# Performance work log

Measured on AMD Instinct MI355X. Metric: run time of the kernel, lower is better.

## Reference

```python
import jax, jax.numpy as jnp
import numpy as np

NUM_GRAPHS = 256


def _mean_aggregate(h, src, dst, num_nodes):
    # DGL copy_src + mean reduce: dst node gets mean of src-node features over in-edges.
    summed = jax.ops.segment_sum(h[src], dst, num_segments=num_nodes)  # [N, F]
    deg = jax.ops.segment_sum(jnp.ones((src.shape[0],), h.dtype), dst, num_segments=num_nodes)
    return summed / jnp.maximum(deg, 1.0)[:, None]


def setup_inputs() -> dict:
    key = jax.random.key(0)
    ks = jax.random.split(key, 10)
    N, E, D_IN, H1, H2, OUT = 50000, 800000, 128, 256, 128, 1
    s = lambda fan: 1.0 / np.sqrt(fan)
    return {
        "h": jax.random.normal(ks[0], (N, D_IN), jnp.float32),
        "src": jax.random.randint(ks[1], (E,), 0, N),
        "dst": jax.random.randint(ks[2], (E,), 0, N),
        "graph_ids": jnp.sort(jax.random.randint(ks[3], (N,), 0, NUM_GRAPHS)),
        "W1": jax.random.normal(ks[4], (D_IN, H1), jnp.float32) * s(D_IN),
        "b1": jnp.zeros((H1,), jnp.float32),
        "W2": jax.random.normal(ks[5], (H1, H1), jnp.float32) * s(H1),
        "b2": jnp.zeros((H1,), jnp.float32),
        "Wr1": jax.random.normal(ks[6], (H1, H2), jnp.float32) * s(H1),
        "br1": jnp.zeros((H2,), jnp.float32),
        "Wr2": jax.random.normal(ks[7], (H2, OUT), jnp.float32) * s(H2),
        "br2": jnp.zeros((OUT,), jnp.float32),
    }


def reference(h, src, dst, graph_ids, W1, b1, W2, b2, Wr1, br1, Wr2, br2):
    N = h.shape[0]
    # GCN layer 1: mean-aggregate then linear+ReLU
    h = _mean_aggregate(h, src, dst, N)
    h = jax.nn.relu(h @ W1 + b1)
    # GCN layer 2
    h = _mean_aggregate(h, src, dst, N)
    h = jax.nn.relu(h @ W2 + b2)
    # dgl.mean_nodes readout: per-graph mean of node features
    gsum = jax.ops.segment_sum(h, graph_ids, num_segments=NUM_GRAPHS)  # [G, H1]
    gcnt = jax.ops.segment_sum(jnp.ones((N,), h.dtype), graph_ids, num_segments=NUM_GRAPHS)
    hg = gsum / jnp.maximum(gcnt, 1.0)[:, None]
    hidden = hg @ Wr1 + br1
    return hidden @ Wr2 + br2  # [G, 1]
```

## Files before the change

kernel.cpp:

```cpp
#include <hip/hip_runtime.h>


#define NUM_GRAPHS 256
#define MAXDEG 64
#define GSHIFT 8
#define GCAP 4864
#define CHUNK_MAX 3200

#define PART_B0 0
#define PART_NB 256
#define CST_B0 (PART_B0 + PART_NB)
#define CST_NB 512
#define GST_B0 (CST_B0 + CST_NB)
#define GST_NB 64
#define WT1_B0 (GST_B0 + GST_NB)
#define WT1_NB 16
#define WT2_B0 (WT1_B0 + WT1_NB)
#define WT2_NB 32
#define MISC_NB (WT2_B0 + WT2_NB)

typedef __attribute__((ext_vector_type(8))) short bf16x8;
typedef __attribute__((ext_vector_type(4))) float f32x4;
typedef __attribute__((ext_vector_type(4))) unsigned int u32x4;

__device__ inline unsigned short f2bf(float f) {
    unsigned u = __float_as_uint(f);
    return (unsigned short)((u + 0x7fff + ((u >> 16) & 1)) >> 16);
}
__device__ inline float bflo(unsigned u) { return __uint_as_float(u << 16); }
__device__ inline float bfhi(unsigned u) { return __uint_as_float(u & 0xffff0000u); }


__launch_bounds__(256)
__global__ void misc_kernel(const int* __restrict__ dst, const int* __restrict__ src,
                            const int* __restrict__ gids,
                            const float* __restrict__ h,
                            const float* __restrict__ W1, const float* __restrict__ W2,
                            int* __restrict__ cursor, unsigned* __restrict__ partE,
                            int* __restrict__ gstart,
                            unsigned short* __restrict__ hb,
                            unsigned short* __restrict__ Wt1, unsigned short* __restrict__ Wt2,
                            int N, int E) {
    int b = blockIdx.x, tid = threadIdx.x;
    if (b < CST_B0) {
        __shared__ unsigned lcnt[256];
        __shared__ unsigned sbuf[256];
        __shared__ unsigned lbase[257];
        __shared__ unsigned gb[256];
        __shared__ unsigned comp[CHUNK_MAX];
        int b0 = b - PART_B0;
        int chunk = (E + PART_NB - 1) / PART_NB;
        int ebeg = b0 * chunk;
        int eend = ebeg + chunk; if (eend > E) eend = E;
        int ecount = eend - ebeg; if (ecount < 0) ecount = 0;

        lcnt[tid] = 0;
        __syncthreads();
        for (int e = ebeg + tid; e < eend; e += 256) {
            int d = __builtin_nontemporal_load(&dst[e]);
            atomicAdd(&lcnt[d >> GSHIFT], 1u);
        }
        __syncthreads();
        unsigned v = lcnt[tid];
        sbuf[tid] = v;
        __syncthreads();
        #pragma unroll
        for (int dd = 1; dd < 256; dd <<= 1) {
            unsigned t = (tid >= dd) ? sbuf[tid - dd] : 0u;
            __syncthreads();
            sbuf[tid] += t;
            __syncthreads();
        }
        lbase[tid] = sbuf[tid] - v;
        if (tid == 255) lbase[256] = sbuf[255];
        gb[tid] = v ? (unsigned)atomicAdd(&cursor[tid], (int)v) : 0u;
        lcnt[tid] = 0;
        __syncthreads();
        for (int e = ebeg + tid; e < eend; e += 256) {
            int d = __builtin_nontemporal_load(&dst[e]);
            int s = __builtin_nontemporal_load(&src[e]);
            int g = d >> GSHIFT;
            unsigned r = atomicAdd(&lcnt[g], 1u) + lbase[g];
            if (r < (unsigned)CHUNK_MAX)
                comp[r] = ((unsigned)s << GSHIFT) | (unsigned)(d & 255);
        }
        __syncthreads();
        for (int i = tid; i < ecount; i += 256) {
            int lo = 0, hi = 256;
            while (hi - lo > 1) {
                int mid = (lo + hi) >> 1;
                if (lbase[mid] <= (unsigned)i) lo = mid; else hi = mid;
            }
            unsigned dest = (unsigned)lo * GCAP + gb[lo] + ((unsigned)i - lbase[lo]);
            if (dest < (unsigned)(256 * GCAP))
                __builtin_nontemporal_store(comp[i], &partE[dest]);
        }
    } else if (b < GST_B0) {
        int lid = (b - CST_B0) * 256 + tid;
        int total4 = N * 32;
        for (int i = lid; i < total4; i += CST_NB * 256) {
            float4 v = *(const float4*)(h + (size_t)i * 4);
            ushort4 o;
            o.x = f2bf(v.x); o.y = f2bf(v.y); o.z = f2bf(v.z); o.w = f2bf(v.w);
            *(ushort4*)(hb + (size_t)i * 4) = o;
        }
    } else if (b < WT1_B0) {
        int lid = (b - GST_B0) * 256 + tid;
        for (int n = lid; n < N; n += GST_NB * 256) {
            int g = gids[n];
            int gp = (n == 0) ? -1 : gids[n - 1];
            for (int x = gp + 1; x <= g; ++x) gstart[x] = n;
            if (n == N - 1)
                for (int x = g + 1; x <= NUM_GRAPHS; ++x) gstart[x] = N;
        }
    } else if (b < WT2_B0) {
        int lid = (b - WT1_B0) * 256 + tid;
        for (int i = lid; i < 256 * 128; i += WT1_NB * 256)
            Wt1[i] = f2bf(W1[(size_t)(i & 127) * 256 + (i >> 7)]);
    } else {
        int lid = (b - WT2_B0) * 256 + tid;
        for (int i = lid; i < 256 * 256; i += WT2_NB * 256)
            Wt2[i] = f2bf(W2[(size_t)(i & 255) * 256 + (i >> 8)]);
    }
}


__launch_bounds__(256)
__global__ void build_kernel(const unsigned* __restrict__ partE,
                             const int* __restrict__ cursor,
                             int* __restrict__ cnt, unsigned short* __restrict__ eidx,
                             int N) {
    __shared__ unsigned short es[256 * MAXDEG];
    __shared__ unsigned hist[256];
    int g = blockIdx.x, tid = threadIdx.x;
    hist[tid] = 0;
    __syncthreads();
    int ec = cursor[g]; if (ec > GCAP) ec = GCAP;
    const unsigned* pe = partE + (size_t)g * GCAP;
    for (int i = tid; i < ec; i += 256) {
        unsigned p = pe[i];
        int dl = (int)(p & 255);
        int s = (int)(p >> GSHIFT);
        unsigned r = atomicAdd(&hist[dl], 1u);
        if (r < MAXDEG)
            es[dl * MAXDEG + r] = (unsigned short)s;
    }
    __syncthreads();
    const u32x4* s4 = (const u32x4*)es;
    u32x4* d4 = (u32x4*)(eidx + ((size_t)g << GSHIFT) * MAXDEG);
    for (int i = tid; i < 2048; i += 256)
        __builtin_nontemporal_store(s4[i], &d4[i]);
    int node = (g << GSHIFT) + tid;
    if (node < N) cnt[node] = (int)hist[tid];
}


template <int D>
__global__ void agg_mean_bf16_kernel(const unsigned short* __restrict__ feat,
                                     const int* __restrict__ cnt,
                                     const unsigned short* __restrict__ eidx,
                                     unsigned short* __restrict__ out, int N) {
    constexpr int VPL = D / 64;
    int wave = blockIdx.x * (blockDim.x >> 6) + (threadIdx.x >> 6);
    int lane = threadIdx.x & 63;
    if (wave >= N) return;
    int deg = cnt[wave];
    int stored = deg > MAXDEG ? MAXDEG : deg;
    const unsigned short* row = eidx + (size_t)wave * MAXDEG;
    int myIdx = (lane < stored) ? (int)row[lane] : 0;

    float acc[VPL];
    #pragma unroll
    for (int i = 0; i < VPL; ++i) acc[i] = 0.0f;

    int j = 0;
    for (; j + 8 <= stored; j += 8) {
        if constexpr (VPL == 2) {
            unsigned v[8];
            #pragma unroll
            for (int u = 0; u < 8; ++u) {
                int s = __shfl(myIdx, j + u, 64);
                v[u] = *(const unsigned*)(feat + (size_t)s * D + lane * 2);
            }
            #pragma unroll
            for (int u = 0; u < 8; ++u) { acc[0] += bflo(v[u]); acc[1] += bfhi(v[u]); }
        } else {
            uint2 v[8];
            #pragma unroll
            for (int u = 0; u < 8; ++u) {
                int s = __shfl(myIdx, j + u, 64);
                v[u] = *(const uint2*)(feat + (size_t)s * D + lane * 4);
            }
            #pragma unroll
            for (int u = 0; u < 8; ++u) {
                acc[0] += bflo(v[u].x); acc[1] += bfhi(v[u].x);
                acc[2] += bflo(v[u].y); acc[3] += bfhi(v[u].y);
            }
        }
    }
    for (; j < stored; ++j) {
        int s = __shfl(myIdx, j, 64);
        if constexpr (VPL == 2) {
            unsigned v = *(const unsigned*)(feat + (size_t)s * D + lane * 2);
            acc[0] += bflo(v); acc[1] += bfhi(v);
        } else {
            uint2 v = *(const uint2*)(feat + (size_t)s * D + lane * 4);
            acc[0] += bflo(v.x); acc[1] += bfhi(v.x);
            acc[2] += bflo(v.y); acc[3] += bfhi(v.y);
        }
    }

    float invd = 1.0f / (float)(deg > 0 ? deg : 1);
    if constexpr (VPL == 2) {
        unsigned o = (unsigned)f2bf(acc[0] * invd) | ((unsigned)f2bf(acc[1] * invd) << 16);
        __builtin_nontemporal_store(o, (unsigned*)(out + (size_t)wave * D + lane * 2));
    } else {
        unsigned lo = (unsigned)f2bf(acc[0] * invd) | ((unsigned)f2bf(acc[1] * invd) << 16);
        unsigned hi = (unsigned)f2bf(acc[2] * invd) | ((unsigned)f2bf(acc[3] * invd) << 16);
        unsigned long long o = (unsigned long long)lo | ((unsigned long long)hi << 32);
        __builtin_nontemporal_store(o, (unsigned long long*)(out + (size_t)wave * D + lane * 4));
    }
}


template <int K, int MODE>
__launch_bounds__(256)
__global__ void gemm_mfma_kernel(const unsigned short* __restrict__ A,
                                 const unsigned short* __restrict__ Wt,
                                 const float* __restrict__ bias,
                                 unsigned short* __restrict__ Cb,
                                 const int* __restrict__ gids,
                                 float* __restrict__ gsum,
                                 int N) {
    constexpr int LDS = 40;
    __shared__ unsigned short As[64 * LDS];
    __shared__ unsigned short Bs[256 * LDS];

    int tid = threadIdx.x;
    int wave = tid >> 6;
    int lane = tid & 63;
    int m = lane & 15;
    int q = lane >> 4;
    int rowBase = blockIdx.x * 64;

    f32x4 acc[4][4] = {};

    for (int kc = 0; kc < K; kc += 32) {
        {
            int r = tid >> 2;
            int seg = tid & 3;
            int gr = rowBase + r;
            uint4 v = make_uint4(0, 0, 0, 0);
            if (gr < N) v = *(const uint4*)(A + (size_t)gr * K + kc + seg * 8);
            *(uint4*)&As[r * LDS + seg * 8] = v;
        }
        #pragma unroll
        for (int it = 0; it < 4; ++it) {
            int n = (tid >> 2) + it * 64;
            int seg = tid & 3;
            uint4 v = *(const uint4*)(Wt + (size_t)n * K + kc + seg * 8);
            *(uint4*)&Bs[n * LDS + seg * 8] = v;
        }
        __syncthreads();

        bf16x8 af[4], bfr[4];
        #pragma unroll
        for (int r = 0; r < 4; ++r)
            af[r] = *(const bf16x8*)&As[(r * 16 + m) * LDS + q * 8];
        #pragma unroll
        for (int c = 0; c < 4; ++c)
            bfr[c] = *(const bf16x8*)&Bs[(wave * 64 + c * 16 + m) * LDS + q * 8];
        #pragma unroll
        for (int r = 0; r < 4; ++r)
            #pragma unroll
            for (int c = 0; c < 4; ++c)
                acc[r][c] = __builtin_amdgcn_mfma_f32_16x16x32_bf16(af[r], bfr[c], acc[r][c], 0, 0, 0);
        __syncthreads();
    }

    if constexpr (MODE == 0) {
        #pragma unroll
        for (int c = 0; c < 4; ++c) {
            int col = wave * 64 + c * 16 + m;
            float bv = bias[col];
            #pragma unroll
            for (int r = 0; r < 4; ++r) {
                #pragma unroll
                for (int reg = 0; reg < 4; ++reg) {
                    int grow = rowBase + r * 16 + q * 4 + reg;
                    if (grow < N)
                        Cb[(size_t)grow * 256 + col] = f2bf(fmaxf(acc[r][c][reg] + bv, 0.0f));
                }
            }
        }
    } else {
        int* sgid = (int*)As;
        if (tid < 64) {
            int gr = rowBase + tid;
            sgid[tid] = (gr < N) ? gids[gr] : 0x7fffffff;
        }
        __syncthreads();
        int lastValid = N - 1 - rowBase;
        if (lastValid > 63) lastValid = 63;
        int gmin = sgid[0];
        int gmax = sgid[lastValid];
        #pragma unroll
        for (int c = 0; c < 4; ++c) {
            int col = wave * 64 + c * 16 + m;
            float bv = bias[col];
            for (int g = gmin; g <= gmax; ++g) {
                float p = 0.0f;
                #pragma unroll
                for (int r = 0; r < 4; ++r) {
                    #pragma unroll
                    for (int reg = 0; reg < 4; ++reg) {
                        int lr = r * 16 + q * 4 + reg;
                        if (sgid[lr] == g)
                            p += fmaxf(acc[r][c][reg] + bv, 0.0f);
                    }
                }
                p += __shfl_xor(p, 16, 64);
                p += __shfl_xor(p, 32, 64);
                if (q == 0 && p != 0.0f)
                    atomicAdd(&gsum[g * 256 + col], p);
            }
        }
    }
}


__global__ void final_kernel(const float* __restrict__ gsum, const int* __restrict__ gstart,
                             const float* __restrict__ Wr1, const float* __restrict__ br1,
                             const float* __restrict__ Wr2, const float* __restrict__ br2,
                             float* __restrict__ out) {
    __shared__ float part[512];
    __shared__ float ws2[2];
    int g = blockIdx.x;
    int t = threadIdx.x;
    int j = t & 127;
    int kq = t >> 7;
    int c = gstart[g + 1] - gstart[g];
    float invc = 1.0f / (float)(c > 0 ? c : 1);
    const float* gs = gsum + g * 256;
    float acc = 0.0f;
    #pragma unroll 8
    for (int k = kq * 64; k < kq * 64 + 64; ++k)
        acc += gs[k] * Wr1[k * 128 + j];
    part[t] = acc;
    __syncthreads();
    if (t < 128) {
        float s = part[j] + part[128 + j] + part[256 + j] + part[384 + j];
        float p = (s * invc + br1[j]) * Wr2[j];
        #pragma unroll
        for (int d = 32; d > 0; d >>= 1) p += __shfl_down(p, d, 64);
        if ((t & 63) == 0) ws2[t >> 6] = p;
    }
    __syncthreads();
    if (t == 0) out[g] = ws2[0] + ws2[1] + br2[0];
}


extern "C" void kernel_launch(void* const* d_in, const int* in_sizes, int n_in,
                              void* d_out, int out_size, void* d_ws, size_t ws_size,
                              hipStream_t stream) {
    const float* h    = (const float*)d_in[0];
    const int*   src  = (const int*)d_in[1];
    const int*   dst  = (const int*)d_in[2];
    const int*   gids = (const int*)d_in[3];
    const float* W1   = (const float*)d_in[4];
    const float* b1   = (const float*)d_in[5];
    const float* W2   = (const float*)d_in[6];
    const float* b2   = (const float*)d_in[7];
    const float* Wr1  = (const float*)d_in[8];
    const float* br1  = (const float*)d_in[9];
    const float* Wr2  = (const float*)d_in[10];
    const float* br2  = (const float*)d_in[11];

    int N = in_sizes[0] / 128;
    int E = in_sizes[1];
    int ngrp = (N + 255) >> GSHIFT;

    char* w = (char*)d_ws;
    unsigned short* hb     = (unsigned short*)w;  w += (size_t)N * 128 * sizeof(unsigned short);
    unsigned short* h1b    = (unsigned short*)w;  w += (size_t)N * 256 * sizeof(unsigned short);
    unsigned short* aggOut = (unsigned short*)w;  w += (size_t)N * 256 * sizeof(unsigned short);
    int* cnt    = (int*)w;              w += (size_t)N * sizeof(int);
    float* gsum = (float*)w;            w += (size_t)NUM_GRAPHS * 256 * sizeof(float);
    int* cursor = (int*)w;              w += 256 * sizeof(int);
    unsigned short* eidx = (unsigned short*)w;  w += (size_t)ngrp * 256 * MAXDEG * sizeof(unsigned short);
    unsigned short* Wt1 = (unsigned short*)w;   w += 256 * 128 * sizeof(unsigned short);
    unsigned short* Wt2 = (unsigned short*)w;   w += 256 * 256 * sizeof(unsigned short);
    int* gstart = (int*)w;              w += (size_t)(NUM_GRAPHS + 1) * sizeof(int);
    unsigned* partE = (unsigned*)aggOut;

    (void)hipMemsetAsync(gsum, 0,
                         (size_t)NUM_GRAPHS * 256 * sizeof(float) + 256 * sizeof(int),
                         stream);
    misc_kernel<<<MISC_NB, 256, 0, stream>>>(dst, src, gids, h, W1, W2, cursor, partE,
                                             gstart, hb, Wt1, Wt2, N, E);
    build_kernel<<<ngrp, 256, 0, stream>>>(partE, cursor, cnt, eidx, N);

    agg_mean_bf16_kernel<128><<<(N + 3) / 4, 256, 0, stream>>>(hb, cnt, eidx, aggOut, N);
    gemm_mfma_kernel<128, 0><<<(N + 63) / 64, 256, 0, stream>>>(aggOut, Wt1, b1, h1b, nullptr, nullptr, N);

    agg_mean_bf16_kernel<256><<<(N + 3) / 4, 256, 0, stream>>>(h1b, cnt, eidx, aggOut, N);
    gemm_mfma_kernel<256, 1><<<(N + 63) / 64, 256, 0, stream>>>(aggOut, Wt2, b2, nullptr, gids, gsum, N);

    final_kernel<<<NUM_GRAPHS, 512, 0, stream>>>(gsum, gstart, Wr1, br1, Wr2, br2, (float*)d_out);
}
```

Measured before the change: 279.4 us.

## Replace global cursor atomics with per-block slices and fuse final readout into GEMM

The edge partition no longer does global atomicAdd cursors. Each partition block writes its per-bucket count to a bcnt matrix and its edges into a fixed BCAP slice, and the build kernel rebuilds offsets with a prefix scan plus binary search. The memset is removed: gsum and the done counter are zeroed inside the first GEMM. The final readout kernel is folded into the second GEMM's tail through a grid-wide done counter with spin-waiting. This saves two launches and the global atomic contention, but the spin-wait can deadlock if the graph-readout blocks are resident while later blocks cannot be scheduled, and BCAP=48 truncates buckets that receive more edges.

```diff
diff --git a/kernel.cpp b/kernel.cpp
--- a/kernel.cpp
+++ b/kernel.cpp
@@ -4,7 +4,8 @@
 #define NUM_GRAPHS 256
 #define MAXDEG 64
 #define GSHIFT 8
-#define GCAP 4864
+#define BCAP 48
+#define GSLICE (256 * BCAP)
 #define CHUNK_MAX 3200
 
 #define PART_B0 0
@@ -36,7 +37,7 @@
                             const int* __restrict__ gids,
                             const float* __restrict__ h,
                             const float* __restrict__ W1, const float* __restrict__ W2,
-                            int* __restrict__ cursor, unsigned* __restrict__ partE,
+                            int* __restrict__ bcnt, unsigned* __restrict__ partE,
                             int* __restrict__ gstart,
                             unsigned short* __restrict__ hb,
                             unsigned short* __restrict__ Wt1, unsigned short* __restrict__ Wt2,
@@ -46,7 +47,6 @@
         __shared__ unsigned lcnt[256];
         __shared__ unsigned sbuf[256];
         __shared__ unsigned lbase[257];
-        __shared__ unsigned gb[256];
         __shared__ unsigned comp[CHUNK_MAX];
         int b0 = b - PART_B0;
         int chunk = (E + PART_NB - 1) / PART_NB;
@@ -73,7 +73,7 @@
         }
         lbase[tid] = sbuf[tid] - v;
         if (tid == 255) lbase[256] = sbuf[255];
-        gb[tid] = v ? (unsigned)atomicAdd(&cursor[tid], (int)v) : 0u;
+        bcnt[b0 * 256 + tid] = (int)(v < BCAP ? v : BCAP);
         lcnt[tid] = 0;
         __syncthreads();
         for (int e = ebeg + tid; e < eend; e += 256) {
@@ -91,9 +91,10 @@
                 int mid = (lo + hi) >> 1;
                 if (lbase[mid] <= (unsigned)i) lo = mid; else hi = mid;
             }
-            unsigned dest = (unsigned)lo * GCAP + gb[lo] + ((unsigned)i - lbase[lo]);
-            if (dest < (unsigned)(256 * GCAP))
-                __builtin_nontemporal_store(comp[i], &partE[dest]);
+            unsigned off = (unsigned)i - lbase[lo];
+            if (off < (unsigned)BCAP)
+                __builtin_nontemporal_store(
+                    comp[i], &partE[(size_t)lo * GSLICE + (unsigned)b0 * BCAP + off]);
         }
     } else if (b < GST_B0) {
         int lid = (b - CST_B0) * 256 + tid;
@@ -127,18 +128,36 @@
 
 __launch_bounds__(256)
 __global__ void build_kernel(const unsigned* __restrict__ partE,
-                             const int* __restrict__ cursor,
+                             const int* __restrict__ bcnt,
                              int* __restrict__ cnt, unsigned short* __restrict__ eidx,
                              int N) {
     __shared__ unsigned short es[256 * MAXDEG];
     __shared__ unsigned hist[256];
+    __shared__ unsigned sb[256];
+    __shared__ unsigned bpre[257];
     int g = blockIdx.x, tid = threadIdx.x;
     hist[tid] = 0;
+    unsigned v = (unsigned)bcnt[tid * 256 + g];
+    sb[tid] = v;
     __syncthreads();
-    int ec = cursor[g]; if (ec > GCAP) ec = GCAP;
-    const unsigned* pe = partE + (size_t)g * GCAP;
-    for (int i = tid; i < ec; i += 256) {
-        unsigned p = pe[i];
+    #pragma unroll
+    for (int dd = 1; dd < 256; dd <<= 1) {
+        unsigned t = (tid >= dd) ? sb[tid - dd] : 0u;
+        __syncthreads();
+        sb[tid] += t;
+        __syncthreads();
+    }
+    bpre[tid] = sb[tid] - v;
+    if (tid == 255) bpre[256] = sb[255];
+    __syncthreads();
+    int tot = (int)bpre[256];
+    for (int f = tid; f < tot; f += 256) {
+        int lo = 0, hi = 256;
+        while (hi - lo > 1) {
+            int mid = (lo + hi) >> 1;
+            if (bpre[mid] <= (unsigned)f) lo = mid; else hi = mid;
+        }
+        unsigned p = partE[(size_t)g * GSLICE + (unsigned)lo * BCAP + ((unsigned)f - bpre[lo])];
         int dl = (int)(p & 255);
         int s = (int)(p >> GSHIFT);
         unsigned r = atomicAdd(&hist[dl], 1u);
@@ -231,7 +250,10 @@
                                  unsigned short* __restrict__ Cb,
                                  const int* __restrict__ gids,
                                  float* __restrict__ gsum,
-                                 int N) {
+                                 int N, int* __restrict__ done,
+                                 const float* __restrict__ Wr1, const float* __restrict__ br1,
+                                 const float* __restrict__ Wr2, const float* __restrict__ br2,
+                                 const int* __restrict__ gstart, float* __restrict__ out) {
     constexpr int LDS = 40;
     __shared__ unsigned short As[64 * LDS];
     __shared__ unsigned short Bs[256 * LDS];
@@ -242,6 +264,11 @@
     int m = lane & 15;
     int q = lane >> 4;
     int rowBase = blockIdx.x * 64;
+
+    if constexpr (MODE == 0) {
+        if (blockIdx.x < NUM_GRAPHS) gsum[blockIdx.x * 256 + tid] = 0.0f;
+        if (blockIdx.x == 0 && tid == 0) *done = 0;
+    }
 
     f32x4 acc[4][4] = {};
 
@@ -325,38 +352,40 @@
                     atomicAdd(&gsum[g * 256 + col], p);
             }
         }
-    }
-}
-
-
-__global__ void final_kernel(const float* __restrict__ gsum, const int* __restrict__ gstart,
-                             const float* __restrict__ Wr1, const float* __restrict__ br1,
-                             const float* __restrict__ Wr2, const float* __restrict__ br2,
-                             float* __restrict__ out) {
-    __shared__ float part[512];
-    __shared__ float ws2[2];
-    int g = blockIdx.x;
-    int t = threadIdx.x;
-    int j = t & 127;
-    int kq = t >> 7;
-    int c = gstart[g + 1] - gstart[g];
-    float invc = 1.0f / (float)(c > 0 ? c : 1);
-    const float* gs = gsum + g * 256;
-    float acc = 0.0f;
-    #pragma unroll 8
-    for (int k = kq * 64; k < kq * 64 + 64; ++k)
-        acc += gs[k] * Wr1[k * 128 + j];
-    part[t] = acc;
-    __syncthreads();
-    if (t < 128) {
-        float s = part[j] + part[128 + j] + part[256 + j] + part[384 + j];
-        float p = (s * invc + br1[j]) * Wr2[j];
-        #pragma unroll
-        for (int d = 32; d > 0; d >>= 1) p += __shfl_down(p, d, 64);
-        if ((t & 63) == 0) ws2[t >> 6] = p;
-    }
-    __syncthreads();
-    if (t == 0) out[g] = ws2[0] + ws2[1] + br2[0];
+        __threadfence();
+        if (tid == 0) atomicAdd(done, 1);
+        if (blockIdx.x < NUM_GRAPHS) {
+            __shared__ float sgs[256];
+            __shared__ float part[256];
+            __shared__ float ws2h[2];
+            if (tid == 0) {
+                while (atomicAdd(done, 0) < (int)gridDim.x) {}
+            }
+            __syncthreads();
+            int g = blockIdx.x;
+            sgs[tid] = atomicAdd(&gsum[g * 256 + tid], 0.0f);
+            __syncthreads();
+            int c = gstart[g + 1] - gstart[g];
+            float invc = 1.0f / (float)(c > 0 ? c : 1);
+            int j = tid & 127;
+            int kq = tid >> 7;
+            float acch = 0.0f;
+            #pragma unroll 8
+            for (int k = kq * 128; k < kq * 128 + 128; ++k)
+                acch += sgs[k] * Wr1[k * 128 + j];
+            part[tid] = acch;
+            __syncthreads();
+            if (tid < 128) {
+                float s2 = part[j] + part[128 + j];
+                float p = (s2 * invc + br1[j]) * Wr2[j];
+                #pragma unroll
+                for (int d = 32; d > 0; d >>= 1) p += __shfl_down(p, d, 64);
+                if ((tid & 63) == 0) ws2h[tid >> 6] = p;
+            }
+            __syncthreads();
+            if (tid == 0) out[g] = ws2h[0] + ws2h[1] + br2[0];
+        }
+    }
 }
 
 
@@ -386,25 +415,25 @@
     unsigned short* aggOut = (unsigned short*)w;  w += (size_t)N * 256 * sizeof(unsigned short);
     int* cnt    = (int*)w;              w += (size_t)N * sizeof(int);
     float* gsum = (float*)w;            w += (size_t)NUM_GRAPHS * 256 * sizeof(float);
-    int* cursor = (int*)w;              w += 256 * sizeof(int);
+    int* done   = (int*)w;              w += 16;
+    int* bcnt   = (int*)w;              w += 256 * 256 * sizeof(int);
     unsigned short* eidx = (unsigned short*)w;  w += (size_t)ngrp * 256 * MAXDEG * sizeof(unsigned short);
     unsigned short* Wt1 = (unsigned short*)w;   w += 256 * 128 * sizeof(unsigned short);
     unsigned short* Wt2 = (unsigned short*)w;   w += 256 * 256 * sizeof(unsigned short);
     int* gstart = (int*)w;              w += (size_t)(NUM_GRAPHS + 1) * sizeof(int);
     unsigned* partE = (unsigned*)aggOut;
 
-    (void)hipMemsetAsync(gsum, 0,
-                         (size_t)NUM_GRAPHS * 256 * sizeof(float) + 256 * sizeof(int),
-                         stream);
-    misc_kernel<<<MISC_NB, 256, 0, stream>>>(dst, src, gids, h, W1, W2, cursor, partE,
+    misc_kernel<<<MISC_NB, 256, 0, stream>>>(dst, src, gids, h, W1, W2, bcnt, partE,
                                              gstart, hb, Wt1, Wt2, N, E);
-    build_kernel<<<ngrp, 256, 0, stream>>>(partE, cursor, cnt, eidx, N);
+    build_kernel<<<ngrp, 256, 0, stream>>>(partE, bcnt, cnt, eidx, N);
 
     agg_mean_bf16_kernel<128><<<(N + 3) / 4, 256, 0, stream>>>(hb, cnt, eidx, aggOut, N);
-    gemm_mfma_kernel<128, 0><<<(N + 63) / 64, 256, 0, stream>>>(aggOut, Wt1, b1, h1b, nullptr, nullptr, N);
+    gemm_mfma_kernel<128, 0><<<(N + 63) / 64, 256, 0, stream>>>(
+        aggOut, Wt1, b1, h1b, nullptr, gsum, N, done,
+        nullptr, nullptr, nullptr, nullptr, nullptr, nullptr);
 
     agg_mean_bf16_kernel<256><<<(N + 3) / 4, 256, 0, stream>>>(h1b, cnt, eidx, aggOut, N);
-    gemm_mfma_kernel<256, 1><<<(N + 63) / 64, 256, 0, stream>>>(aggOut, Wt2, b2, nullptr, gids, gsum, N);
-
-    final_kernel<<<NUM_GRAPHS, 512, 0, stream>>>(gsum, gstart, Wr1, br1, Wr2, br2, (float*)d_out);
-}
+    gemm_mfma_kernel<256, 1><<<(N + 63) / 64, 256, 0, stream>>>(
+        aggOut, Wt2, b2, nullptr, gids, gsum, N, done,
+        Wr1, br1, Wr2, br2, gstart, (float*)d_out);
+}
```

Measured after the change: 395.7 us. 41.6% more time.
